# Performance work log

Hardware: AMD Instinct MI355X
Metric: run time of the kernel (lower is better)

Reference implementation:

```python
import jax, jax.numpy as jnp
import numpy as np

RADIUS = 2
TOP_K = 4096
TEMPERATURE = 0.1
KSIZE = 2 * RADIUS + 1  # 5


def _max_pool(x, r):
    k = 2 * r + 1
    return jax.lax.reduce_window(x, -jnp.inf, jax.lax.max,
                                 (1, 1, k, k), (1, 1, 1, 1), 'SAME')


def simple_nms(scores, r):
    zeros = jnp.zeros_like(scores)
    max_mask = scores == _max_pool(scores, r)
    for _ in range(2):
        supp_mask = _max_pool(max_mask.astype(scores.dtype), r) > 0
        supp_scores = jnp.where(supp_mask, zeros, scores)
        new_max_mask = supp_scores == _max_pool(supp_scores, r)
        max_mask = max_mask | (new_max_mask & ~supp_mask)
    return jnp.where(max_mask, scores, zeros)


def _bilinear_sample(img, px, py):
    # grid_sample, mode=bilinear, padding_mode=zeros, align_corners=True.
    # img: [H, W]; px, py: pixel coords [K]
    H, W = img.shape
    x0 = jnp.floor(px); y0 = jnp.floor(py)
    wx1 = px - x0; wx0 = 1.0 - wx1
    wy1 = py - y0; wy0 = 1.0 - wy1

    def g(xf, yf):
        xi = jnp.clip(xf.astype(jnp.int32), 0, W - 1)
        yi = jnp.clip(yf.astype(jnp.int32), 0, H - 1)
        valid = (xf >= 0) & (xf <= W - 1) & (yf >= 0) & (yf <= H - 1)
        return jnp.where(valid, img[yi, xi], 0.0)

    return (wy0 * wx0 * g(x0, y0) + wy0 * wx1 * g(x0 + 1, y0)
            + wy1 * wx0 * g(x0, y0 + 1) + wy1 * wx1 * g(x0 + 1, y0 + 1))


def setup_inputs() -> dict:
    key = jax.random.key(0)
    scores_map = jax.random.uniform(key, (8, 1, 1024, 1024), dtype=jnp.float32)
    return {'scores_map': scores_map}


def reference(scores_map):
    b, c, H, W = scores_map.shape
    r = RADIUS

    scores_nograd = jax.lax.stop_gradient(scores_map)
    nms = simple_nms(scores_nograd, r)
    # zero the borders (image_size is None)
    nms = nms.at[:, :, :r, :].set(0.0)
    nms = nms.at[:, :, :, :r].set(0.0)
    nms = nms.at[:, :, -r:, :].set(0.0)
    nms = nms.at[:, :, :, -r:].set(0.0)

    # top_k > 0 branch: fixed-size selection per image
    _, idx = jax.lax.top_k(nms.reshape(b, -1), TOP_K)  # [B, K]
    rows = idx // W
    cols = idx % W

    # soft-argmax offset grid: (dx, dy) pairs, row-major over the 5x5 patch
    lin = jnp.linspace(-r, r, KSIZE, dtype=scores_map.dtype)
    gi, gj = jnp.meshgrid(lin, lin, indexing='ij')
    hw_grid = jnp.stack([gj.reshape(-1), gi.reshape(-1)], axis=-1)  # [25, 2]

    # gather 5x5 patches at keypoints (equivalent to unfold + row-index)
    oi, oj = jnp.meshgrid(jnp.arange(KSIZE), jnp.arange(KSIZE), indexing='ij')
    oi = oi.reshape(-1); oj = oj.reshape(-1)  # [25]
    padded = jnp.pad(scores_map[:, 0], ((0, 0), (r, r), (r, r)))  # zero pad like Unfold

    def gather_patches(pad_s, rr, cc):
        return pad_s[rr[:, None] + oi[None, :], cc[:, None] + oj[None, :]]  # [K, 25]

    patches = jax.vmap(gather_patches)(padded, rows, cols)  # [B, K, 25]

    max_v = jax.lax.stop_gradient(patches.max(axis=-1, keepdims=True))
    x_exp = jnp.exp((patches - max_v) / TEMPERATURE)  # [B, K, 25]
    ssum = x_exp.sum(axis=-1)  # [B, K]
    xy_residual = jnp.einsum('bkp,pc->bkc', x_exp, hw_grid) / ssum[..., None]

    diff = (hw_grid[None, None, :, :] - xy_residual[:, :, None, :]) / r
    hw_grid_dist2 = jnp.sum(diff * diff, axis=-1)  # [B, K, 25]
    scoredispersity = jnp.sum(x_exp * hw_grid_dist2, axis=-1) / ssum  # [B, K]

    kpts_nms = jnp.stack([cols, rows], axis=-1).astype(scores_map.dtype)  # (x, y)
    wh = jnp.array([W - 1, H - 1], dtype=scores_map.dtype)
    keypoints_xy = (kpts_nms + xy_residual) / wh * 2.0 - 1.0  # [B, K, 2] in [-1, 1]

    # grid_sample lookup of the (differentiable) score map at sub-pixel locations
    px = (keypoints_xy[..., 0] + 1.0) * 0.5 * (W - 1)
    py = (keypoints_xy[..., 1] + 1.0) * 0.5 * (H - 1)
    kptscores = jax.vmap(_bilinear_sample)(scores_map[:, 0], px, py)  # [B, K]

    return keypoints_xy, scoredispersity, kptscores
```

## Files before the change

### kernel.cpp

```cpp
#include <hip/hip_runtime.h>

typedef unsigned int u32;
typedef unsigned long long u64;

#define B 8
#define H 1024
#define W 1024
#define TOPK 4096
#define CANDCAP 131072
#define GCAP 8192
#define LBUFW 320
#define CSTR 32
#define NB2 8192
#define HPAD 8200
#define BAND 4096

__device__ __forceinline__ float max3(float a, float b, float c) {
    float r;
    asm("v_max3_f32 %0, %1, %2, %3" : "=v"(r) : "v"(a), "v"(b), "v"(c));
    return r;
}
#define MAX5R(A, j) max3(max3(A[j], A[(j)+1], A[(j)+2]), A[(j)+3], A[(j)+4])
#define OR5(A, j) (A[j] | A[(j)+1] | A[(j)+2] | A[(j)+3] | A[(j)+4])

__device__ __forceinline__ u32 bkt(u32 vb) {
    if (vb < 0x3F000000u) return 0u;
    u32 b = ((vb - 0x3F000000u) >> 10) + 1u;
    return b > NB2 ? NB2 : b;
}

__device__ __forceinline__ u64 xdilate(u64 m) {
    return m | (m << 1) | (m >> 1) | (m << 2) | (m >> 2);
}

__device__ __forceinline__ float xmax5(float v) {
    float u1 = __shfl_up(v, 1), d1 = __shfl_down(v, 1);
    float u2 = __shfl_up(v, 2), d2 = __shfl_down(v, 2);
    return max3(max3(v, u1, d1), u2, d2);
}

__device__ __forceinline__ float selz(u64 m, float v) {
    float r;
    asm("v_cndmask_b32 %0, %1, 0, %2" : "=v"(r) : "v"(v), "s"(m));
    return r;
}
__device__ __forceinline__ float selnz(u64 m, float v) {
    float r;
    asm("v_cndmask_b32 %0, 0, %1, %2" : "=v"(r) : "v"(v), "s"(m));
    return r;
}


__global__ __launch_bounds__(256, 4) void k_nms(const float* __restrict__ S_,
                                                u64* __restrict__ cand,
                                                u32* __restrict__ cnt,
                                                u32* __restrict__ hist) {
    __shared__ u64 lbuf[4][LBUFW];

    int lane = threadIdx.x & 63;
    int wslot = threadIdx.x >> 6;
    int sx = blockIdx.x * 4 + wslot;
    int sy = blockIdx.y;
    int img = blockIdx.z;

    {
        int bid = blockIdx.x + 6 * blockIdx.y;
        u32 base = (u32)bid * 43u;
        u32* gh = hist + (u32)img * HPAD;
        int t0 = threadIdx.x;
        if (t0 < 43 && base + t0 < HPAD) gh[base + t0] = 0;
    }

    int gx0 = sx * 44 - 10;
    int gy0 = sy * 32;
    int gx = gx0 + lane;
    bool lxok = (unsigned)gx < (unsigned)W;
    u64 lanebit = 1ull << lane;
    const float* Sb = S_ + ((size_t)img << 20);

    u64 validx = __ballot(lxok);
    u64 emask = __ballot(lane >= 10 && lane <= 53 && gx >= 2 && gx <= W - 3);

    float S[14], R0[8], R1[8], R2[8], nxt[4];
    u64 M0[8], M1[8], SP1[6], SP2[6];
#pragma unroll
    for (int k = 0; k < 14; ++k) S[k] = -1.0f;
#pragma unroll
    for (int k = 0; k < 8; ++k) { R0[k] = -1e30f; R1[k] = -1e30f; R2[k] = -1e30f; M0[k] = 0; M1[k] = 0; }
#pragma unroll
    for (int k = 0; k < 6; ++k) { SP1[k] = 0; SP2[k] = 0; }

    u32 wbase = 0;
    int y0 = gy0 - 10;

#pragma unroll
    for (int j = 0; j < 4; ++j) {
        int gy = y0 + j;
        nxt[j] = ((unsigned)gy < (unsigned)H && lxok) ? Sb[(gy << 10) + gx] : -1.0f;
    }

    for (int cy = 0; cy < 13; ++cy, y0 += 4) {
#pragma unroll
        for (int j = 0; j < 4; ++j) S[10 + j] = nxt[j];
        if (cy < 12) {
#pragma unroll
            for (int j = 0; j < 4; ++j) {
                int gy = y0 + 4 + j;
                nxt[j] = ((unsigned)gy < (unsigned)H && lxok) ? Sb[(gy << 10) + gx] : -1.0f;
            }
        }
#pragma unroll
        for (int j = 0; j < 4; ++j) {
            R0[4 + j] = xmax5(S[10 + j]);
            float c0 = MAX5R(R0, j);
            u64 m0 = __ballot(S[j + 8] == c0) & validx;
            M0[4 + j] = m0;

            u64 sp1 = xdilate(OR5(M0, j));
            SP1[2 + j] = sp1;

            float ss1 = selz(sp1, S[j + 6]);
            R1[4 + j] = xmax5(ss1);
            float c1 = MAX5R(R1, j);
            float ss1b = selz(SP1[j], S[j + 4]);
            u64 new1 = __ballot(ss1b == c1) & validx;
            u64 m1 = M0[j] | (new1 & ~SP1[j]);
            M1[4 + j] = m1;

            u64 sp2 = xdilate(OR5(M1, j));
            SP2[2 + j] = sp2;

            float ss2 = selz(sp2, S[j + 2]);
            R2[4 + j] = xmax5(ss2);

            if (cy >= 5) {
                float c2 = MAX5R(R2, j);
                float ss2b = selz(SP2[j], S[j]);
                u64 new2 = __ballot(ss2b == c2) & validx;
                u64 m2 = M1[j] | (new2 & ~SP2[j]);
                int gy_out = y0 + j - 10;
                if (gy_out >= 2 && gy_out <= H - 3) {
                    float val = selnz(m2, S[j]);
                    u64 bm = __ballot(val > 0.0f) & emask;
                    if (bm) {
                        u32 cw = (u32)__popcll(bm);
                        u32 prefix = (u32)__popcll(bm & (lanebit - 1ull));
                        if ((bm & lanebit) && (wbase + prefix) < LBUFW) {
                            u64 key = (((u64)__float_as_uint(val)) << 32) |
                                      (u32)(~(u32)((gy_out << 10) + gx));
                            lbuf[wslot][wbase + prefix] = key;
                        }
                        wbase += cw;
                    }
                }
            }
        }
#pragma unroll
        for (int k = 0; k < 10; ++k) S[k] = S[k + 4];
#pragma unroll
        for (int k = 0; k < 4; ++k) {
            R0[k] = R0[k + 4]; R1[k] = R1[k + 4]; R2[k] = R2[k + 4];
            M0[k] = M0[k + 4]; M1[k] = M1[k + 4];
        }
#pragma unroll
        for (int k = 0; k < 2; ++k) { SP1[k] = SP1[k + 4]; SP2[k] = SP2[k + 4]; }
    }

    u32 total = wbase > LBUFW ? LBUFW : wbase;
    u32 gbase = 0;
    if (lane == 0) gbase = atomicAdd(&cnt[img * CSTR], total);
    gbase = (u32)__shfl((int)gbase, 0, 64);
    u64* dst = cand + ((size_t)img << 17);
    for (u32 i = lane; i < total; i += 64)
        dst[gbase + i] = lbuf[wslot][i];
}


__global__ __launch_bounds__(256) void k_hist(const u64* __restrict__ cand,
                                              const u32* __restrict__ cnt,
                                              u32* __restrict__ hist) {
    __shared__ u32 h[NB2 + 1];
    int img = blockIdx.y;
    int t = threadIdx.x;
    for (int i = t; i <= NB2; i += 256) h[i] = 0;
    __syncthreads();
    u32 n = cnt[img * CSTR];
    if (n > CANDCAP) n = CANDCAP;
    const u64* c = cand + ((size_t)img << 17);
    u32 per = (n + gridDim.x - 1) / gridDim.x;
    u32 lo = blockIdx.x * per;
    u32 hiX = lo + per; if (hiX > n) hiX = n;
    for (u32 i = lo + t; i < hiX; i += 256)
        atomicAdd(&h[bkt((u32)(c[i] >> 32))], 1u);
    __syncthreads();
    u32* gh = hist + (u32)img * HPAD;
    for (int i = t; i <= NB2; i += 256)
        if (h[i]) atomicAdd(&gh[i], h[i]);
}


__global__ __launch_bounds__(1024) void k_scan(const u32* __restrict__ hist,
                                               u32* __restrict__ dparr,
                                               u32* __restrict__ dpcnt,
                                               u32* __restrict__ Bsr,
                                               u32* __restrict__ gtot) {
    __shared__ u32 wpart[16], woff[16];
    __shared__ u32 sBs, sGc;
    int img = blockIdx.x, t = threadIdx.x;
    int lane = t & 63, wid = t >> 6;
    const u32* h = hist + (u32)img * HPAD;
    int hi = NB2 - 8 * t;
    u32 loc[8];
    u32 psum = 0;
#pragma unroll
    for (int i = 0; i < 8; ++i) { loc[i] = h[hi - i]; psum += loc[i]; }
    u32 incl = psum;
#pragma unroll
    for (int d = 1; d < 64; d <<= 1) {
        u32 x = (u32)__shfl_up((int)incl, d);
        if (lane >= d) incl += x;
    }
    if (lane == 63) wpart[wid] = incl;
    if (t == 0) { sBs = 0; sGc = 0; }
    __syncthreads();
    if (t == 0) { u32 a = 0; for (int w2 = 0; w2 < 16; ++w2) { woff[w2] = a; a += wpart[w2]; } }
    __syncthreads();
    u32 total1 = woff[15] + wpart[15];
    u32 excl = incl - psum + woff[wid];

    u32* dpi = dparr + (u32)img * HPAD;
    u32* dci = dpcnt + (u32)img * HPAD;
    u32 dpv = excl;
#pragma unroll
    for (int i = 0; i < 8; ++i) {
        dpi[hi - i] = dpv;
        dci[hi - i] = dpv;
        dpv += loc[i];
    }
    if (t == 1023) { dpi[0] = dpv; dci[0] = dpv; }
    if (excl < TOPK && excl + psum >= TOPK) {
        u32 cum = excl;
#pragma unroll
        for (int i = 0; i < 8; ++i) {
            cum += loc[i];
            if (cum >= TOPK) { sBs = (u32)(hi - i); sGc = cum; break; }
        }
    }
    __syncthreads();
    if (t == 0) {
        u32 bs = sBs, gc = sGc;
        if (total1 < TOPK) { bs = 0; gc = total1 + h[0]; }
        Bsr[img * CSTR] = bs;
        gtot[img * CSTR] = gc > GCAP ? GCAP : gc;
    }
}


__global__ __launch_bounds__(256) void k_gather(const u64* __restrict__ cand,
                                                const u32* __restrict__ cnt,
                                                const u32* __restrict__ Bsr,
                                                u32* __restrict__ dpcnt,
                                                u64* __restrict__ gath) {
    __shared__ u32 hb[BAND];
    __shared__ u32 ho[BAND];
    int img = blockIdx.y, t = threadIdx.x;
    for (int i = t; i < BAND; i += 256) hb[i] = 0;
    __syncthreads();
    u32 n = cnt[img * CSTR];
    if (n > CANDCAP) n = CANDCAP;
    u32 Bs = Bsr[img * CSTR];
    const u64* c = cand + ((size_t)img << 17);
    u32* dci = dpcnt + (u32)img * HPAD;
    u32 per = (n + gridDim.x - 1) / gridDim.x;
    u32 lo = blockIdx.x * per;
    u32 hiX = lo + per; if (hiX > n) hiX = n;

    for (u32 i = lo + t; i < hiX; i += 256) {
        u32 b = bkt((u32)(c[i] >> 32));
        if (b >= Bs) {
            u32 idx = b - Bs;
            if (idx < BAND) atomicAdd(&hb[idx], 1u);
        }
    }
    __syncthreads();
    for (int i = t; i < BAND; i += 256) {
        u32 cv = hb[i];
        if (cv) { ho[i] = atomicAdd(&dci[Bs + i], cv); hb[i] = 0; }
    }
    __syncthreads();
    u64* g = gath + ((size_t)img << 13);
    for (u32 i = lo + t; i < hiX; i += 256) {
        u64 key = c[i];
        u32 b = bkt((u32)(key >> 32));
        if (b < Bs) continue;
        u32 idx = b - Bs;
        u32 pos;
        if (idx < BAND) pos = ho[idx] + atomicAdd(&hb[idx], 1u);
        else pos = atomicAdd(&dci[b], 1u);
        if (pos < GCAP) g[pos] = key;
    }
}


__global__ __launch_bounds__(256) void k_rankfinal(const u64* __restrict__ gath,
                                                   const u32* __restrict__ gtot,
                                                   const u32* __restrict__ dparr,
                                                   const float* __restrict__ S,
                                                   float* __restrict__ out) {
    int img = blockIdx.y;
    u32 n = gtot[img * CSTR];
    if (n > GCAP) n = GCAP;
    u32 i = blockIdx.x * 256 + threadIdx.x;
    if (i >= n) return;
    const u64* g = gath + ((size_t)img << 13);
    u64 key = g[i];
    u32 b = bkt((u32)(key >> 32));
    const u32* dpi = dparr + (u32)img * HPAD;
    u32 lo = dpi[b];
    u32 hiE = (b >= 1) ? dpi[b - 1] : n;
    if (hiE > n) hiE = n;
    u32 r = lo;
    for (u32 j = lo; j < hiE; ++j) r += (g[j] > key);
    if (r >= TOPK) return;

    u32 rem = ~(u32)(key & 0xFFFFFFFFull);
    int row = (int)(rem >> 10);
    int col = (int)(rem & (W - 1));
    const float* Sb = S + ((size_t)img << 20);

    float p[25];
    float mx = -1e30f;
#pragma unroll
    for (int a2 = 0; a2 < 5; ++a2) {
        int y = row + a2 - 2;
#pragma unroll
        for (int c2 = 0; c2 < 5; ++c2) {
            int x = col + c2 - 2;
            float v = (y >= 0 && y < H && x >= 0 && x < W) ? Sb[(y << 10) + x] : 0.0f;
            p[a2 * 5 + c2] = v;
            mx = fmaxf(mx, v);
        }
    }
    float sum = 0.0f, sx = 0.0f, sy = 0.0f;
#pragma unroll
    for (int a2 = 0; a2 < 5; ++a2) {
#pragma unroll
        for (int c2 = 0; c2 < 5; ++c2) {
            float e = expf((p[a2 * 5 + c2] - mx) / 0.1f);
            p[a2 * 5 + c2] = e;
            sum += e;
            sx += e * (float)(c2 - 2);
            sy += e * (float)(a2 - 2);
        }
    }
    float rx = sx / sum, ry = sy / sum;
    float sd = 0.0f;
#pragma unroll
    for (int a2 = 0; a2 < 5; ++a2) {
#pragma unroll
        for (int c2 = 0; c2 < 5; ++c2) {
            float dxx = ((float)(c2 - 2) - rx) * 0.5f;
            float dyy = ((float)(a2 - 2) - ry) * 0.5f;
            sd += p[a2 * 5 + c2] * (dxx * dxx + dyy * dyy);
        }
    }
    float disp = sd / sum;
    float kx = ((float)col + rx) / (float)(W - 1) * 2.0f - 1.0f;
    float ky = ((float)row + ry) / (float)(H - 1) * 2.0f - 1.0f;

    float px = (kx + 1.0f) * 0.5f * (float)(W - 1);
    float py = (ky + 1.0f) * 0.5f * (float)(H - 1);
    float x0 = floorf(px), y0 = floorf(py);
    float wx1 = px - x0, wx0 = 1.0f - wx1;
    float wy1 = py - y0, wy0 = 1.0f - wy1;

    float gg[4];
    float xs[4] = {x0, x0 + 1.0f, x0, x0 + 1.0f};
    float ys[4] = {y0, y0, y0 + 1.0f, y0 + 1.0f};
#pragma unroll
    for (int q = 0; q < 4; ++q) {
        int xi = (int)xs[q]; xi = xi < 0 ? 0 : (xi > W - 1 ? W - 1 : xi);
        int yi = (int)ys[q]; yi = yi < 0 ? 0 : (yi > H - 1 ? H - 1 : yi);
        bool valid = (xs[q] >= 0.0f) && (xs[q] <= (float)(W - 1)) &&
                     (ys[q] >= 0.0f) && (ys[q] <= (float)(H - 1));
        gg[q] = valid ? Sb[(yi << 10) + xi] : 0.0f;
    }
    float score = wy0 * wx0 * gg[0] + wy0 * wx1 * gg[1] + wy1 * wx0 * gg[2] + wy1 * wx1 * gg[3];

    u32 slot = ((u32)img << 12) + r;
    out[(size_t)slot * 2]     = kx;
    out[(size_t)slot * 2 + 1] = ky;
    out[B * TOPK * 2 + slot]            = disp;
    out[B * TOPK * 2 + B * TOPK + slot] = score;
}


extern "C" void kernel_launch(void* const* d_in, const int* in_sizes, int n_in,
                              void* d_out, int out_size, void* d_ws, size_t ws_size,
                              hipStream_t stream) {
    const float* S = (const float*)d_in[0];
    float* out = (float*)d_out;

    char* w = (char*)d_ws;
    u64* cand = (u64*)w;        w += (size_t)B * CANDCAP * 8;
    u64* gath = (u64*)w;        w += (size_t)B * GCAP * 8;
    u32* hist = (u32*)w;        w += (size_t)B * HPAD * 4;
    u32* cnt = (u32*)w;         w += B * CSTR * 4;
    u32* dparr = (u32*)w;       w += (size_t)B * HPAD * 4;
    u32* dpcnt = (u32*)w;       w += (size_t)B * HPAD * 4;
    u32* Bsr = (u32*)w;         w += B * CSTR * 4;
    u32* gtot = (u32*)w;        w += B * CSTR * 4;

    hipMemsetAsync(cnt, 0, B * CSTR * 4, stream);

    k_nms<<<dim3(6, 32, B), 256, 0, stream>>>(S, cand, cnt, hist);
    k_hist<<<dim3(16, B), 256, 0, stream>>>(cand, cnt, hist);
    k_scan<<<B, 1024, 0, stream>>>(hist, dparr, dpcnt, Bsr, gtot);
    k_gather<<<dim3(16, B), 256, 0, stream>>>(cand, cnt, Bsr, dpcnt, gath);
    k_rankfinal<<<dim3(32, B), 256, 0, stream>>>(gath, gtot, dparr, S, out);
}
```

Measured before the change: 114.6 us.

## Use fixed per-wave candidate slabs and fuse histogram with last-block scan

```diff
diff --git a/kernel.cpp b/kernel.cpp
--- a/kernel.cpp
+++ b/kernel.cpp
@@ -7,9 +7,9 @@
 #define H 1024
 #define W 1024
 #define TOPK 4096
-#define CANDCAP 131072
 #define GCAP 8192
 #define LBUFW 320
+#define NSLAB 768
 #define CSTR 32
 #define NB2 8192
 #define HPAD 8200
@@ -53,8 +53,9 @@
 
 __global__ __launch_bounds__(256, 4) void k_nms(const float* __restrict__ S_,
                                                 u64* __restrict__ cand,
-                                                u32* __restrict__ cnt,
-                                                u32* __restrict__ hist) {
+                                                u32* __restrict__ bcnt,
+                                                u32* __restrict__ hist,
+                                                u32* __restrict__ done) {
     __shared__ u64 lbuf[4][LBUFW];
 
     int lane = threadIdx.x & 63;
@@ -62,13 +63,14 @@
     int sx = blockIdx.x * 4 + wslot;
     int sy = blockIdx.y;
     int img = blockIdx.z;
+    int bid = blockIdx.x + 6 * blockIdx.y;
 
     {
-        int bid = blockIdx.x + 6 * blockIdx.y;
         u32 base = (u32)bid * 43u;
         u32* gh = hist + (u32)img * HPAD;
         int t0 = threadIdx.x;
         if (t0 < 43 && base + t0 < HPAD) gh[base + t0] = 0;
+        if (bid == 0 && t0 == 0) done[img * CSTR] = 0;
     }
 
     int gx0 = sx * 44 - 10;
@@ -167,53 +169,69 @@
     }
 
     u32 total = wbase > LBUFW ? LBUFW : wbase;
-    u32 gbase = 0;
-    if (lane == 0) gbase = atomicAdd(&cnt[img * CSTR], total);
-    gbase = (u32)__shfl((int)gbase, 0, 64);
-    u64* dst = cand + ((size_t)img << 17);
+    int slab = bid * 4 + wslot;
+    u64* dst = cand + ((size_t)img << 18) + (size_t)slab * LBUFW;
     for (u32 i = lane; i < total; i += 64)
-        dst[gbase + i] = lbuf[wslot][i];
-}
-
-
-__global__ __launch_bounds__(256) void k_hist(const u64* __restrict__ cand,
-                                              const u32* __restrict__ cnt,
-                                              u32* __restrict__ hist) {
+        dst[i] = lbuf[wslot][i];
+    if (lane == 0) bcnt[img * NSLAB + slab] = total;
+}
+
+
+__global__ __launch_bounds__(256) void k_histscan(const u64* __restrict__ cand,
+                                                  const u32* __restrict__ bcnt,
+                                                  u32* __restrict__ hist,
+                                                  u32* __restrict__ done,
+                                                  u32* __restrict__ dparr,
+                                                  u32* __restrict__ dpcnt,
+                                                  u32* __restrict__ Bsr,
+                                                  u32* __restrict__ gtot) {
     __shared__ u32 h[NB2 + 1];
+    __shared__ u32 wpart[4], woff[4];
+    __shared__ u32 sflag, sBs, sGc, sH0;
     int img = blockIdx.y;
     int t = threadIdx.x;
+
     for (int i = t; i <= NB2; i += 256) h[i] = 0;
     __syncthreads();
-    u32 n = cnt[img * CSTR];
-    if (n > CANDCAP) n = CANDCAP;
-    const u64* c = cand + ((size_t)img << 17);
-    u32 per = (n + gridDim.x - 1) / gridDim.x;
-    u32 lo = blockIdx.x * per;
-    u32 hiX = lo + per; if (hiX > n) hiX = n;
-    for (u32 i = lo + t; i < hiX; i += 256)
-        atomicAdd(&h[bkt((u32)(c[i] >> 32))], 1u);
-    __syncthreads();
+
+    const u64* c = cand + ((size_t)img << 18);
+    for (int s = 0; s < NSLAB / 16; ++s) {
+        int slab = blockIdx.x * (NSLAB / 16) + s;
+        u32 n = bcnt[img * NSLAB + slab];
+        if (n > LBUFW) n = LBUFW;
+        const u64* cs = c + (size_t)slab * LBUFW;
+        for (u32 i = t; i < n; i += 256)
+            atomicAdd(&h[bkt((u32)(cs[i] >> 32))], 1u);
+    }
+    __syncthreads();
+
     u32* gh = hist + (u32)img * HPAD;
-    for (int i = t; i <= NB2; i += 256)
-        if (h[i]) atomicAdd(&gh[i], h[i]);
-}
-
-
-__global__ __launch_bounds__(1024) void k_scan(const u32* __restrict__ hist,
-                                               u32* __restrict__ dparr,
-                                               u32* __restrict__ dpcnt,
-                                               u32* __restrict__ Bsr,
-                                               u32* __restrict__ gtot) {
-    __shared__ u32 wpart[16], woff[16];
-    __shared__ u32 sBs, sGc;
-    int img = blockIdx.x, t = threadIdx.x;
+    for (int i = t; i <= NB2; i += 256) {
+        u32 v = h[i];
+        if (v) atomicAdd(&gh[i], v);
+    }
+    __threadfence();
+    __syncthreads();
+    if (t == 0) {
+        u32 prev = atomicAdd(&done[img * CSTR], 1u);
+        sflag = (prev == 15) ? 1u : 0u;
+        sBs = 0; sGc = 0;
+    }
+    __syncthreads();
+    if (!sflag) return;
+    __threadfence();
+
     int lane = t & 63, wid = t >> 6;
-    const u32* h = hist + (u32)img * HPAD;
-    int hi = NB2 - 8 * t;
-    u32 loc[8];
+    int hi = NB2 - 32 * t;
+    u32 loc[32];
     u32 psum = 0;
 #pragma unroll
-    for (int i = 0; i < 8; ++i) { loc[i] = h[hi - i]; psum += loc[i]; }
+    for (int i = 0; i < 32; ++i) {
+        loc[i] = __hip_atomic_load(&gh[hi - i], __ATOMIC_RELAXED, __HIP_MEMORY_SCOPE_AGENT);
+        psum += loc[i];
+    }
+    if (t == 255)
+        sH0 = __hip_atomic_load(&gh[0], __ATOMIC_RELAXED, __HIP_MEMORY_SCOPE_AGENT);
     u32 incl = psum;
 #pragma unroll
     for (int d = 1; d < 64; d <<= 1) {
@@ -221,27 +239,26 @@
         if (lane >= d) incl += x;
     }
     if (lane == 63) wpart[wid] = incl;
-    if (t == 0) { sBs = 0; sGc = 0; }
-    __syncthreads();
-    if (t == 0) { u32 a = 0; for (int w2 = 0; w2 < 16; ++w2) { woff[w2] = a; a += wpart[w2]; } }
-    __syncthreads();
-    u32 total1 = woff[15] + wpart[15];
+    __syncthreads();
+    if (t == 0) { u32 a = 0; for (int w2 = 0; w2 < 4; ++w2) { woff[w2] = a; a += wpart[w2]; } }
+    __syncthreads();
+    u32 total1 = woff[3] + wpart[3];
     u32 excl = incl - psum + woff[wid];
 
     u32* dpi = dparr + (u32)img * HPAD;
     u32* dci = dpcnt + (u32)img * HPAD;
     u32 dpv = excl;
 #pragma unroll
-    for (int i = 0; i < 8; ++i) {
+    for (int i = 0; i < 32; ++i) {
         dpi[hi - i] = dpv;
         dci[hi - i] = dpv;
         dpv += loc[i];
     }
-    if (t == 1023) { dpi[0] = dpv; dci[0] = dpv; }
+    if (t == 255) { dpi[0] = dpv; dci[0] = dpv; }
     if (excl < TOPK && excl + psum >= TOPK) {
         u32 cum = excl;
 #pragma unroll
-        for (int i = 0; i < 8; ++i) {
+        for (int i = 0; i < 32; ++i) {
             cum += loc[i];
             if (cum >= TOPK) { sBs = (u32)(hi - i); sGc = cum; break; }
         }
@@ -249,7 +266,7 @@
     __syncthreads();
     if (t == 0) {
         u32 bs = sBs, gc = sGc;
-        if (total1 < TOPK) { bs = 0; gc = total1 + h[0]; }
+        if (total1 < TOPK) { bs = 0; gc = total1 + sH0; }
         Bsr[img * CSTR] = bs;
         gtot[img * CSTR] = gc > GCAP ? GCAP : gc;
     }
@@ -257,7 +274,7 @@
 
 
 __global__ __launch_bounds__(256) void k_gather(const u64* __restrict__ cand,
-                                                const u32* __restrict__ cnt,
+                                                const u32* __restrict__ bcnt,
                                                 const u32* __restrict__ Bsr,
                                                 u32* __restrict__ dpcnt,
                                                 u64* __restrict__ gath) {
@@ -266,20 +283,21 @@
     int img = blockIdx.y, t = threadIdx.x;
     for (int i = t; i < BAND; i += 256) hb[i] = 0;
     __syncthreads();
-    u32 n = cnt[img * CSTR];
-    if (n > CANDCAP) n = CANDCAP;
     u32 Bs = Bsr[img * CSTR];
-    const u64* c = cand + ((size_t)img << 17);
+    const u64* c = cand + ((size_t)img << 18);
     u32* dci = dpcnt + (u32)img * HPAD;
-    u32 per = (n + gridDim.x - 1) / gridDim.x;
-    u32 lo = blockIdx.x * per;
-    u32 hiX = lo + per; if (hiX > n) hiX = n;
-
-    for (u32 i = lo + t; i < hiX; i += 256) {
-        u32 b = bkt((u32)(c[i] >> 32));
-        if (b >= Bs) {
-            u32 idx = b - Bs;
-            if (idx < BAND) atomicAdd(&hb[idx], 1u);
+
+    for (int s = 0; s < NSLAB / 16; ++s) {
+        int slab = blockIdx.x * (NSLAB / 16) + s;
+        u32 n = bcnt[img * NSLAB + slab];
+        if (n > LBUFW) n = LBUFW;
+        const u64* cs = c + (size_t)slab * LBUFW;
+        for (u32 i = t; i < n; i += 256) {
+            u32 b = bkt((u32)(cs[i] >> 32));
+            if (b >= Bs) {
+                u32 idx = b - Bs;
+                if (idx < BAND) atomicAdd(&hb[idx], 1u);
+            }
         }
     }
     __syncthreads();
@@ -289,15 +307,21 @@
     }
     __syncthreads();
     u64* g = gath + ((size_t)img << 13);
-    for (u32 i = lo + t; i < hiX; i += 256) {
-        u64 key = c[i];
-        u32 b = bkt((u32)(key >> 32));
-        if (b < Bs) continue;
-        u32 idx = b - Bs;
-        u32 pos;
-        if (idx < BAND) pos = ho[idx] + atomicAdd(&hb[idx], 1u);
-        else pos = atomicAdd(&dci[b], 1u);
-        if (pos < GCAP) g[pos] = key;
+    for (int s = 0; s < NSLAB / 16; ++s) {
+        int slab = blockIdx.x * (NSLAB / 16) + s;
+        u32 n = bcnt[img * NSLAB + slab];
+        if (n > LBUFW) n = LBUFW;
+        const u64* cs = c + (size_t)slab * LBUFW;
+        for (u32 i = t; i < n; i += 256) {
+            u64 key = cs[i];
+            u32 b = bkt((u32)(key >> 32));
+            if (b < Bs) continue;
+            u32 idx = b - Bs;
+            u32 pos;
+            if (idx < BAND) pos = ho[idx] + atomicAdd(&hb[idx], 1u);
+            else pos = atomicAdd(&dci[b], 1u);
+            if (pos < GCAP) g[pos] = key;
+        }
     }
 }
 
@@ -402,20 +426,19 @@
     float* out = (float*)d_out;
 
     char* w = (char*)d_ws;
-    u64* cand = (u64*)w;        w += (size_t)B * CANDCAP * 8;
+    u64* cand = (u64*)w;        w += (size_t)B * (1 << 18) * 8;
     u64* gath = (u64*)w;        w += (size_t)B * GCAP * 8;
     u32* hist = (u32*)w;        w += (size_t)B * HPAD * 4;
-    u32* cnt = (u32*)w;         w += B * CSTR * 4;
     u32* dparr = (u32*)w;       w += (size_t)B * HPAD * 4;
     u32* dpcnt = (u32*)w;       w += (size_t)B * HPAD * 4;
+    u32* bcnt = (u32*)w;        w += (size_t)B * NSLAB * 4;
+    u32* done = (u32*)w;        w += B * CSTR * 4;
     u32* Bsr = (u32*)w;         w += B * CSTR * 4;
     u32* gtot = (u32*)w;        w += B * CSTR * 4;
 
-    hipMemsetAsync(cnt, 0, B * CSTR * 4, stream);
-
-    k_nms<<<dim3(6, 32, B), 256, 0, stream>>>(S, cand, cnt, hist);
-    k_hist<<<dim3(16, B), 256, 0, stream>>>(cand, cnt, hist);
-    k_scan<<<B, 1024, 0, stream>>>(hist, dparr, dpcnt, Bsr, gtot);
-    k_gather<<<dim3(16, B), 256, 0, stream>>>(cand, cnt, Bsr, dpcnt, gath);
+
+    k_nms<<<dim3(6, 32, B), 256, 0, stream>>>(S, cand, bcnt, hist, done);
+    k_histscan<<<dim3(16, B), 256, 0, stream>>>(cand, bcnt, hist, done, dparr, dpcnt, Bsr, gtot);
+    k_gather<<<dim3(16, B), 256, 0, stream>>>(cand, bcnt, Bsr, dpcnt, gath);
     k_rankfinal<<<dim3(32, B), 256, 0, stream>>>(gath, gtot, dparr, S, out);
 }
```

Result: slower. 142.1 us, median of 3 (+24.0%).
